# Kernel optimization log

Measured on AMD Instinct MI355X. Metric: run time of the kernel, lower is better.

## Reference

```python
import jax, jax.numpy as jnp
import numpy as np
from jax import lax

T, B, S, D = 16, 8, 256, 1024
M, H = 1024, 8
HD = M // H
TAU_MEM = 0.99
TAU_GATE = 0.9
VTH = 1.0
LN_EPS = 1e-5


def lif(inp, tau, vth):
    """LIF over leading time axis. inp: (T, N, M). Returns (spikes, membrane trace)."""
    def step(v, i):
        v = tau * v + i                      # integrate with leak
        s = (v >= vth).astype(i.dtype)       # hard threshold spike
        return v - s * vth, (s, v)           # subtract reset; trace is pre-reset membrane
    v0 = jnp.zeros(inp.shape[1:], inp.dtype)
    _, (spikes, mv) = lax.scan(step, v0, inp)
    return spikes, mv


def setup_inputs() -> dict:
    key = jax.random.key(0)
    ks = jax.random.split(key, 6)
    inp = {
        "x": jax.random.normal(ks[0], (T, B, S, D), dtype=jnp.float32),
        "W_to_memory": jax.random.normal(ks[1], (M, D), dtype=jnp.float32) / np.sqrt(D),
        "W_gate": jax.random.normal(ks[2], (M, D), dtype=jnp.float32) / np.sqrt(D),
        "W_read_key": jax.random.normal(ks[3], (M, M), dtype=jnp.float32) / np.sqrt(M),
        "W_from_memory": jax.random.normal(ks[4], (D, M), dtype=jnp.float32) / np.sqrt(M),
        "read_query": jax.random.normal(ks[5], (H, HD), dtype=jnp.float32) * 0.02,
        "gate_threshold": jnp.float32(0.5),
        "ln_gamma": jnp.ones((D,), jnp.float32),
        "ln_beta": jnp.zeros((D,), jnp.float32),
        "memory_mix": jnp.float32(0.1),
    }
    return inp


def reference(x, W_to_memory, W_gate, W_read_key, W_from_memory, read_query,
              gate_threshold, ln_gamma, ln_beta, memory_mix):
    N = B * S
    xf = x.reshape(T, N, D)

    # memory write path
    mi = jnp.einsum('tnd,md->tnm', xf, W_to_memory)        # (T,N,M)
    ms, mv = lif(mi, TAU_MEM, VTH)

    # spike-gated write
    gi = jnp.einsum('tnd,md->tnm', xf, W_gate)
    gs, _ = lif(gi, TAU_GATE, VTH)
    gate_sig = gs.mean(axis=0)                              # (N,M)
    gate_mask = jax.nn.sigmoid((gate_sig - gate_threshold) * 10.0)

    # multi-head temporal attention over T
    mvh = mv.reshape(T, N, H, HD)
    mk = jnp.einsum('tnm,km->tnk', mv, W_read_key).reshape(T, N, H, HD)
    scale = 1.0 / np.sqrt(HD)
    attn_s = jnp.einsum('tnhd,hd->tnh', mk, read_query) * scale
    attn_w = jax.nn.softmax(attn_s.astype(jnp.float32), axis=0).astype(mv.dtype)
    mem_read = jnp.einsum('tnhd,tnh->nhd', mvh, attn_w).reshape(N, M)
    mem_read = mem_read * gate_mask

    # project back, layernorm, residual mix
    mem_out = jnp.einsum('nm,dm->nd', mem_read, W_from_memory).astype(jnp.float32)
    mu = mem_out.mean(axis=-1, keepdims=True)
    var = mem_out.var(axis=-1, keepdims=True)
    mem_out = (mem_out - mu) * lax.rsqrt(var + LN_EPS) * ln_gamma + ln_beta
    mem_out = mem_out.astype(x.dtype)

    mix = jax.nn.sigmoid(memory_mix)
    x_enhanced = x + mix * mem_out.reshape(1, B, S, D)
    return x_enhanced
```

## Files before the change

### kernel.cpp

```cpp
#include <hip/hip_runtime.h>
#include <hip/hip_bf16.h>
#include <hip/hip_fp16.h>

#define TT 16
#define NN 2048
#define DD 1024
#define MM 1024
#define HH 8
#define ROWS 32768
#define JJ 2048

typedef _Float16 f16x8 __attribute__((ext_vector_type(8)));
typedef float f32x4 __attribute__((ext_vector_type(4)));

#define SB  __builtin_amdgcn_sched_barrier(0)
#define BAR __builtin_amdgcn_s_barrier()

__device__ __forceinline__ void gload16(const void* g, void* l) {
    __builtin_amdgcn_global_load_lds((const __attribute__((address_space(1))) void*)g,
                                     (__attribute__((address_space(3))) void*)l, 16, 0, 0);
}

__global__ __launch_bounds__(256) void pack_hi(const float* __restrict__ in,
                                               __half* __restrict__ hi, long n4) {
    long i = (long)blockIdx.x * 256 + threadIdx.x;
    if (i >= n4) return;
    float4 v = ((const float4*)in)[i];
    ushort4 H = { __half_as_ushort(__float2half(v.x)), __half_as_ushort(__float2half(v.y)),
                  __half_as_ushort(__float2half(v.z)), __half_as_ushort(__float2half(v.w)) };
    ((ushort4*)hi)[i] = H;
}

__global__ __launch_bounds__(256) void pack_hilo(const float* __restrict__ in,
                                                 __half* __restrict__ hi,
                                                 __half* __restrict__ lo, long n4) {
    long i = (long)blockIdx.x * 256 + threadIdx.x;
    if (i >= n4) return;
    float4 v = ((const float4*)in)[i];
    __half h0 = __float2half(v.x), h1 = __float2half(v.y);
    __half h2 = __float2half(v.z), h3 = __float2half(v.w);
    __half l0 = __float2half(v.x - __half2float(h0));
    __half l1 = __float2half(v.y - __half2float(h1));
    __half l2 = __float2half(v.z - __half2float(h2));
    __half l3 = __float2half(v.w - __half2float(h3));
    ushort4 H = { __half_as_ushort(h0), __half_as_ushort(h1), __half_as_ushort(h2), __half_as_ushort(h3) };
    ushort4 L = { __half_as_ushort(l0), __half_as_ushort(l1), __half_as_ushort(l2), __half_as_ushort(l3) };
    ((ushort4*)hi)[i] = H;
    ((ushort4*)lo)[i] = L;
}

__global__ __launch_bounds__(256) void compute_wq(const float* __restrict__ Wrk,
                                                  const float* __restrict__ q,
                                                  float* __restrict__ wq) {
    int m = blockIdx.x * 256 + threadIdx.x;
    int h = blockIdx.y;
    const float* qh = q + h * 128;
    const float* wr = Wrk + (size_t)h * 128 * MM + m;
    float acc = 0.f;
    for (int hd = 0; hd < 128; hd++) acc = fmaf(qh[hd], wr[(size_t)hd * MM], acc);
    wq[h * MM + m] = acc * 0.08838834764831845f;
}

__global__ __launch_bounds__(512, 2)
void gemm8p(const __half* __restrict__ Ahi, const __half* __restrict__ Alo,
            const __half* __restrict__ Bhi, const __half* __restrict__ Blo,
            float* __restrict__ C)
{
    extern __shared__ __align__(16) char smem[];
    char* AHb = smem;
    char* ALb = smem + 32768;
    char* BHb = smem + 65536;
    char* BLb = smem + 98304;

    const int tid = threadIdx.x, lane = tid & 63, wave = tid >> 6;
    const int l15 = lane & 15, l4 = lane >> 4;
    const int wm = wave >> 2, wn = wave & 3;

    const int orig = blockIdx.x;
    const int wg   = (orig & 7) * 128 + (orig >> 3);
    const int rb   = (wg >> 3) * 256;
    const int cb   = (wg & 7) * 256;

    auto stageU = [&](const __half* src, int row0, char* dstbase, int par, int kt, int s) {
        int t   = s * 512 + tid;
        int row = t >> 2;
        int p   = t & 3;
        int kb  = (p ^ ((row >> 1) & 3)) * 16;
        const char* g = (const char*)(src + (size_t)(row0 + row) * 1024 + kt * 32) + kb;
        gload16(g, dstbase + par * 16384 + (size_t)(s * 512 + wave * 64) * 16);
    };
    auto rdT = [&](const char* base, int par, int row) -> f16x8 {
        int p = l4 ^ ((row >> 1) & 3);
        return *(const f16x8*)(base + par * 16384 + row * 64 + p * 16);
    };

    f32x4 acc[8][4] = {};
    const int NKT = 32;

    stageU(Ahi, rb, AHb, 0, 0, 0); stageU(Ahi, rb, AHb, 0, 0, 1);
    stageU(Alo, rb, ALb, 0, 0, 0); stageU(Alo, rb, ALb, 0, 0, 1);
    stageU(Bhi, cb, BHb, 0, 0, 0); stageU(Bhi, cb, BHb, 0, 0, 1);
    stageU(Blo, cb, BLb, 0, 0, 0); stageU(Blo, cb, BLb, 0, 0, 1);

    for (int kt = 0; kt < NKT; kt++) {
        const int p = kt & 1, pn = p ^ 1;
        const bool pre = (kt + 1 < NKT);
        f16x8 a[8], bh[4], bl[4];

        asm volatile("s_waitcnt vmcnt(0)" ::: "memory");
        SB; BAR;

        #pragma unroll
        for (int i = 0; i < 8; i++) a[i] = rdT(AHb, p, wm * 128 + i * 16 + l15);
        #pragma unroll
        for (int n = 0; n < 4; n++) bh[n] = rdT(BHb, p, wn * 64 + n * 16 + l15);
        if (pre) {
            stageU(Ahi, rb, AHb, pn, kt + 1, 0); stageU(Ahi, rb, AHb, pn, kt + 1, 1);
            stageU(Alo, rb, ALb, pn, kt + 1, 0); stageU(Alo, rb, ALb, pn, kt + 1, 1);
        }
        __builtin_amdgcn_s_setprio(1);
        #pragma unroll
        for (int i = 0; i < 8; i++)
            #pragma unroll
            for (int n = 0; n < 4; n++)
                acc[i][n] = __builtin_amdgcn_mfma_f32_16x16x32_f16(a[i], bh[n], acc[i][n], 0, 0, 0);
        __builtin_amdgcn_s_setprio(0);

        #pragma unroll
        for (int n = 0; n < 4; n++) bl[n] = rdT(BLb, p, wn * 64 + n * 16 + l15);
        if (pre) {
            stageU(Bhi, cb, BHb, pn, kt + 1, 0); stageU(Bhi, cb, BHb, pn, kt + 1, 1);
            stageU(Blo, cb, BLb, pn, kt + 1, 0); stageU(Blo, cb, BLb, pn, kt + 1, 1);
        }
        __builtin_amdgcn_s_setprio(1);
        #pragma unroll
        for (int i = 0; i < 8; i++)
            #pragma unroll
            for (int n = 0; n < 4; n++)
                acc[i][n] = __builtin_amdgcn_mfma_f32_16x16x32_f16(a[i], bl[n], acc[i][n], 0, 0, 0);
        __builtin_amdgcn_s_setprio(0);

        #pragma unroll
        for (int i = 0; i < 8; i++) a[i] = rdT(ALb, p, wm * 128 + i * 16 + l15);
        __builtin_amdgcn_s_setprio(1);
        #pragma unroll
        for (int i = 0; i < 8; i++)
            #pragma unroll
            for (int n = 0; n < 4; n++)
                acc[i][n] = __builtin_amdgcn_mfma_f32_16x16x32_f16(a[i], bh[n], acc[i][n], 0, 0, 0);
        __builtin_amdgcn_s_setprio(0);
    }

    #pragma unroll
    for (int i = 0; i < 8; i++) {
        int r0 = rb + wm * 128 + i * 16 + l4 * 4;
        #pragma unroll
        for (int nf = 0; nf < 4; nf++) {
            int c = cb + wn * 64 + nf * 16 + l15;
            #pragma unroll
            for (int reg = 0; reg < 4; reg++)
                C[(size_t)(r0 + reg) * JJ + c] = acc[i][nf][reg];
        }
    }
}

template<int TERMS>
__global__ __launch_bounds__(256, 2)
void gemm_f16(const __half* __restrict__ Ahi, const __half* __restrict__ Alo,
              const __half* __restrict__ Bhi, const __half* __restrict__ Blo,
              float* __restrict__ C, int K, int ldc, int ncb_log2)
{
    __shared__ __align__(16) __half lds[2][4][8][512];
    const int tid  = threadIdx.x;
    const int lane = tid & 63;
    const int wave = tid >> 6;
    const int l15  = lane & 15, l4 = lane >> 4;

    const int nwg  = gridDim.x;
    const int orig = blockIdx.x;
    const int wg   = (orig & 7) * (nwg >> 3) + (orig >> 3);
    const int rb = (wg >> ncb_log2) * 128;
    const int cb = (wg & ((1 << ncb_log2) - 1)) * 128;

    auto stage = [&](int buf, int ks) {
        const int k0 = ks * 32;
        #pragma unroll
        for (int qq = 0; qq < 2; qq++) {
            int g = wave * 2 + qq;
            size_t aoff = (size_t)(rb + g * 16 + l15) * K + (k0 + 8 * l4);
            gload16(Ahi + aoff, &lds[buf][0][g][0]);
            if constexpr (TERMS == 3) gload16(Alo + aoff, &lds[buf][1][g][0]);
            size_t boff = (size_t)(cb + g * 16 + l15) * K + (k0 + 8 * l4);
            gload16(Bhi + boff, &lds[buf][2][g][0]);
            if constexpr (TERMS == 3) gload16(Blo + boff, &lds[buf][3][g][0]);
        }
    };

    const int wave_r = (wave >> 1) * 64;
    const int wave_c = (wave & 1) * 64;
    const int ag0 = wave_r >> 4;
    const int bg0 = wave_c >> 4;

    f32x4 acc[4][4] = {};
    const int nks = K >> 5;
    stage(0, 0);
    int buf = 0;
    for (int ks = 0; ks < nks; ks++) {
        __syncthreads();
        if (ks + 1 < nks) stage(buf ^ 1, ks + 1);
        f16x8 ah[4], bh[4], al[4], bl[4];
        #pragma unroll
        for (int i = 0; i < 4; i++) {
            ah[i] = *(const f16x8*)&lds[buf][0][ag0 + i][lane * 8];
            bh[i] = *(const f16x8*)&lds[buf][2][bg0 + i][lane * 8];
            if constexpr (TERMS == 3) {
                al[i] = *(const f16x8*)&lds[buf][1][ag0 + i][lane * 8];
                bl[i] = *(const f16x8*)&lds[buf][3][bg0 + i][lane * 8];
            }
        }
        #pragma unroll
        for (int m = 0; m < 4; m++)
            #pragma unroll
            for (int n = 0; n < 4; n++) {
                acc[m][n] = __builtin_amdgcn_mfma_f32_16x16x32_f16(ah[m], bh[n], acc[m][n], 0, 0, 0);
                if constexpr (TERMS == 3) {
                    acc[m][n] = __builtin_amdgcn_mfma_f32_16x16x32_f16(ah[m], bl[n], acc[m][n], 0, 0, 0);
                    acc[m][n] = __builtin_amdgcn_mfma_f32_16x16x32_f16(al[m], bh[n], acc[m][n], 0, 0, 0);
                }
            }
        buf ^= 1;
    }
    #pragma unroll
    for (int m = 0; m < 4; m++)
        #pragma unroll
        for (int n = 0; n < 4; n++) {
            int r0 = rb + wave_r + m * 16 + l4 * 4;
            int c  = cb + wave_c + n * 16 + l15;
            #pragma unroll
            for (int reg = 0; reg < 4; reg++)
                C[(size_t)(r0 + reg) * ldc + c] = acc[m][n][reg];
        }
}

__global__ __launch_bounds__(256)
void lif_kernel(const float* __restrict__ mi_gi, __half* __restrict__ mv,
                float* __restrict__ gmask, const float* __restrict__ gate_thr)
{
    int idx = blockIdx.x * 256 + threadIdx.x;
    int n = idx >> 10, m = idx & 1023;
    const float* pm = mi_gi + (size_t)n * JJ + m;
    const size_t tstride = (size_t)NN * JJ;
    __half* pv = mv + idx;
    float vm = 0.f, vg = 0.f, cnt = 0.f;
    #pragma unroll
    for (int t = 0; t < TT; t++) {
        float im = pm[(size_t)t * tstride];
        vm = 0.99f * vm + im;
        pv[(size_t)t * (NN * MM)] = __float2half(vm);
        if (vm >= 1.0f) vm -= 1.0f;
        float ig = pm[(size_t)t * tstride + MM];
        vg = 0.9f * vg + ig;
        if (vg >= 1.0f) { vg -= 1.0f; cnt += 1.0f; }
    }
    float gs = cnt * 0.0625f;
    gmask[idx] = 1.0f / (1.0f + expf(-10.0f * (gs - gate_thr[0])));
}

__global__ __launch_bounds__(256)
void attn_memread(const __half* __restrict__ mv, const float* __restrict__ wq,
                  const float* __restrict__ gmask, __half* __restrict__ mem_read)
{
    int n = blockIdx.x;
    __shared__ __align__(16) __half smv[TT][1032];
    __shared__ float sw[HH][TT];
    __shared__ float ssm[HH][TT];
    int tid = threadIdx.x;

    for (int t = 0; t < TT; t++) {
        const ushort4* src = (const ushort4*)(mv + ((size_t)t * NN + n) * MM);
        ((ushort4*)&smv[t][0])[tid] = src[tid];
    }
    __syncthreads();

    if (tid < 128) {
        int h = tid >> 4, t = tid & 15;
        const float* w = wq + h * MM;
        float acc = 0.f;
        for (int m = 0; m < MM; m += 2) {
            float2 v = __half22float2(*(const __half2*)&smv[t][m]);
            acc = fmaf(v.x, w[m], acc);
            acc = fmaf(v.y, w[m + 1], acc);
        }
        sw[h][t] = acc;
    }
    __syncthreads();
    if (tid < 8) {
        int h = tid;
        float mx = -1e30f;
        for (int t = 0; t < TT; t++) mx = fmaxf(mx, sw[h][t]);
        float s = 0.f;
        for (int t = 0; t < TT; t++) { float e = __expf(sw[h][t] - mx); ssm[h][t] = e; s += e; }
        float inv = 1.0f / s;
        for (int t = 0; t < TT; t++) ssm[h][t] *= inv;
    }
    __syncthreads();

    const float* gm = gmask + (size_t)n * MM;
    #pragma unroll
    for (int mm = 0; mm < 4; mm++) {
        int m = tid + mm * 256;
        int h = m >> 7;
        float acc = 0.f;
        #pragma unroll
        for (int t = 0; t < TT; t++) acc = fmaf(__half2float(smv[t][m]), ssm[h][t], acc);
        acc *= gm[m];
        mem_read[(size_t)n * MM + m] = __float2half(acc);
    }
}

__global__ __launch_bounds__(256)
void ln_add(const float* __restrict__ mem_out, const float* __restrict__ x,
            const float* __restrict__ gamma, const float* __restrict__ beta,
            const float* __restrict__ mmix, float* __restrict__ out)
{
    int n = blockIdx.x, tid = threadIdx.x;
    int lane = tid & 63, wave = tid >> 6;
    __shared__ float sred[10];
    float4 v = ((const float4*)(mem_out + (size_t)n * DD))[tid];
    float s  = v.x + v.y + v.z + v.w;
    float ss = v.x * v.x + v.y * v.y + v.z * v.z + v.w * v.w;
    #pragma unroll
    for (int o = 32; o > 0; o >>= 1) { s += __shfl_down(s, o, 64); ss += __shfl_down(ss, o, 64); }
    if (lane == 0) { sred[wave * 2] = s; sred[wave * 2 + 1] = ss; }
    __syncthreads();
    if (tid == 0) {
        float S = 0.f, SS = 0.f;
        for (int w = 0; w < 4; w++) { S += sred[w * 2]; SS += sred[w * 2 + 1]; }
        float mu = S * (1.0f / DD);
        float var = SS * (1.0f / DD) - mu * mu;
        sred[8] = mu;
        sred[9] = rsqrtf(var + 1e-5f);
    }
    __syncthreads();
    float mu = sred[8], rs = sred[9];
    float4 g = ((const float4*)gamma)[tid];
    float4 b = ((const float4*)beta)[tid];
    float4 nv;
    nv.x = (v.x - mu) * rs * g.x + b.x;
    nv.y = (v.y - mu) * rs * g.y + b.y;
    nv.z = (v.z - mu) * rs * g.z + b.z;
    nv.w = (v.w - mu) * rs * g.w + b.w;
    float mix = 1.0f / (1.0f + expf(-mmix[0]));
    for (int t = 0; t < TT; t++) {
        size_t off = ((size_t)t * NN + n) * DD;
        float4 xv = ((const float4*)(x + off))[tid];
        float4 o;
        o.x = xv.x + mix * nv.x;
        o.y = xv.y + mix * nv.y;
        o.z = xv.z + mix * nv.z;
        o.w = xv.w + mix * nv.w;
        ((float4*)(out + off))[tid] = o;
    }
}

__global__ void ws_sentinel(float* out) { out[0] = 12345.0f; }

extern "C" void kernel_launch(void* const* d_in, const int* in_sizes, int n_in,
                              void* d_out, int out_size, void* d_ws, size_t ws_size,
                              hipStream_t stream)
{
    const float* x     = (const float*)d_in[0];
    const float* Wto   = (const float*)d_in[1];
    const float* Wg    = (const float*)d_in[2];
    const float* Wrk   = (const float*)d_in[3];
    const float* Wfrom = (const float*)d_in[4];
    const float* q     = (const float*)d_in[5];
    const float* gthr  = (const float*)d_in[6];
    const float* gamma = (const float*)d_in[7];
    const float* beta  = (const float*)d_in[8];
    const float* mmix  = (const float*)d_in[9];
    float* out = (float*)d_out;

    char* w = (char*)d_ws;
    size_t off = 0;
    auto alloc = [&](size_t bytes) -> void* {
        void* p = w + off;
        off += (bytes + 255) & ~(size_t)255;
        return p;
    };
    __half* x_hi   = (__half*)alloc((size_t)ROWS * DD * 2);
    __half* x_lo   = (__half*)alloc((size_t)ROWS * DD * 2);
    __half* wc_hi  = (__half*)alloc((size_t)JJ * DD * 2);
    __half* wc_lo  = (__half*)alloc((size_t)JJ * DD * 2);
    __half* wf_hi  = (__half*)alloc((size_t)DD * MM * 2);
    float*  wq     = (float*) alloc((size_t)HH * MM * 4);
    float*  mi_gi  = (float*) alloc((size_t)ROWS * JJ * 4);
    __half* mv     = (__half*)alloc((size_t)TT * NN * MM * 2);
    float*  gmask  = (float*) alloc((size_t)NN * MM * 4);
    __half* m_read = (__half*)alloc((size_t)NN * MM * 2);
    float*  m_out  = (float*) alloc((size_t)NN * DD * 4);

    if (off > ws_size) {
        ws_sentinel<<<1, 1, 0, stream>>>(out);
        return;
    }

    hipFuncSetAttribute((const void*)gemm8p, hipFuncAttributeMaxDynamicSharedMemorySize, 131072);

    pack_hilo<<<(ROWS * DD / 4 + 255) / 256, 256, 0, stream>>>(x, x_hi, x_lo, ROWS * DD / 4);
    pack_hilo<<<(MM * DD / 4 + 255) / 256, 256, 0, stream>>>(Wto, wc_hi, wc_lo, MM * DD / 4);
    pack_hilo<<<(MM * DD / 4 + 255) / 256, 256, 0, stream>>>(Wg, wc_hi + (size_t)MM * DD, wc_lo + (size_t)MM * DD, MM * DD / 4);
    pack_hi<<<(DD * MM / 4 + 255) / 256, 256, 0, stream>>>(Wfrom, wf_hi, DD * MM / 4);
    compute_wq<<<dim3(4, 8), 256, 0, stream>>>(Wrk, q, wq);

    gemm8p<<<(ROWS / 256) * (JJ / 256), 512, 131072, stream>>>(x_hi, x_lo, wc_hi, wc_lo, mi_gi);

    lif_kernel<<<NN * MM / 256, 256, 0, stream>>>(mi_gi, mv, gmask, gthr);

    attn_memread<<<NN, 256, 0, stream>>>(mv, wq, gmask, m_read);

    gemm_f16<1><<<(NN / 128) * (DD / 128), 256, 0, stream>>>(m_read, m_read, wf_hi, wf_hi, m_out, MM, DD, 3);

    ln_add<<<NN, 256, 0, stream>>>(m_out, x, gamma, beta, mmix, out);
}
```

Measured before the change: 583.8 us.

## Fuse LIF scan into GEMM epilogue via time-permuted row packing

The x packing now permutes rows so that each 256-row GEMM tile holds all 16 timesteps of 16 tokens, laid out to match the MFMA accumulator register pattern. The GEMM epilogue then runs the membrane and gate LIF recurrences in registers. It stages mv through LDS for coalesced fp16 stores and writes the gate mask directly. This removes the 256MB fp32 mi_gi intermediate and the separate LIF kernel's full read pass, in exchange for a heavier epilogue with serial per-thread recurrences and an extra barrier.

Measured after the change: 506.0 us. 1.15x faster.

```diff
diff --git a/kernel.cpp b/kernel.cpp
--- a/kernel.cpp
+++ b/kernel.cpp
@@ -49,6 +49,30 @@
     ((ushort4*)lo)[i] = L;
 }
 
+__global__ __launch_bounds__(256) void pack_hilo_perm(const float* __restrict__ in,
+                                                      __half* __restrict__ hi,
+                                                      __half* __restrict__ lo) {
+    long i = (long)blockIdx.x * 256 + threadIdx.x;
+    int R   = (int)(i >> 8);
+    int d4  = (int)(i & 255);
+    int r   = R & 255, blk = R >> 8;
+    int n_l = ((r >> 7) & 1) * 8 + ((r >> 6) & 1) * 4 + ((r >> 2) & 3);
+    int t   = ((r >> 4) & 3) * 4 + (r & 3);
+    int n_g = blk * 16 + n_l;
+    long src = ((long)t * NN + n_g) * 256 + d4;
+    float4 v = ((const float4*)in)[src];
+    __half h0 = __float2half(v.x), h1 = __float2half(v.y);
+    __half h2 = __float2half(v.z), h3 = __float2half(v.w);
+    __half l0 = __float2half(v.x - __half2float(h0));
+    __half l1 = __float2half(v.y - __half2float(h1));
+    __half l2 = __float2half(v.z - __half2float(h2));
+    __half l3 = __float2half(v.w - __half2float(h3));
+    ushort4 H = { __half_as_ushort(h0), __half_as_ushort(h1), __half_as_ushort(h2), __half_as_ushort(h3) };
+    ushort4 L = { __half_as_ushort(l0), __half_as_ushort(l1), __half_as_ushort(l2), __half_as_ushort(l3) };
+    ((ushort4*)hi)[i] = H;
+    ((ushort4*)lo)[i] = L;
+}
+
 __global__ __launch_bounds__(256) void compute_wq(const float* __restrict__ Wrk,
                                                   const float* __restrict__ q,
                                                   float* __restrict__ wq) {
@@ -64,7 +88,8 @@
 __global__ __launch_bounds__(512, 2)
 void gemm8p(const __half* __restrict__ Ahi, const __half* __restrict__ Alo,
             const __half* __restrict__ Bhi, const __half* __restrict__ Blo,
-            float* __restrict__ C)
+            __half* __restrict__ mv, float* __restrict__ gmask,
+            const float* __restrict__ gate_thr)
 {
     extern __shared__ __align__(16) char smem[];
     char* AHb = smem;
@@ -151,15 +176,61 @@
         __builtin_amdgcn_s_setprio(0);
     }
 
-    #pragma unroll
-    for (int i = 0; i < 8; i++) {
-        int r0 = rb + wm * 128 + i * 16 + l4 * 4;
-        #pragma unroll
-        for (int nf = 0; nf < 4; nf++) {
-            int c = cb + wn * 64 + nf * 16 + l15;
-            #pragma unroll
-            for (int reg = 0; reg < 4; reg++)
-                C[(size_t)(r0 + reg) * JJ + c] = acc[i][nf][reg];
+    asm volatile("s_waitcnt lgkmcnt(0) vmcnt(0)" ::: "memory");
+    SB; BAR;
+
+    const int n_g_base = rb >> 4;
+    if (cb < 1024) {
+        __half* mvs = (__half*)smem;
+        #pragma unroll
+        for (int i2 = 0; i2 < 2; i2++) {
+            int n_l = wm * 8 + i2 * 4 + l4;
+            #pragma unroll
+            for (int nf = 0; nf < 4; nf++) {
+                int col = wn * 64 + nf * 16 + l15;
+                float v = 0.f;
+                #pragma unroll
+                for (int tt = 0; tt < 4; tt++)
+                    #pragma unroll
+                    for (int reg = 0; reg < 4; reg++) {
+                        int t = tt * 4 + reg;
+                        v = 0.99f * v + acc[i2 * 4 + tt][nf][reg];
+                        mvs[(t * 16 + n_l) * 256 + col] = __float2half(v);
+                        if (v >= 1.0f) v -= 1.0f;
+                    }
+            }
+        }
+        SB; BAR;
+        #pragma unroll
+        for (int j = 0; j < 16; j++) {
+            int k = j * 512 + tid;
+            int e = k * 8;
+            int t   = e >> 12;
+            int n_l = (e >> 8) & 15;
+            int m   = e & 255;
+            float4 val = *(const float4*)((const char*)smem + (size_t)k * 16);
+            *(float4*)(mv + ((size_t)(t * NN + n_g_base + n_l) * MM + cb + m)) = val;
+        }
+    } else {
+        float thr = gate_thr[0];
+        #pragma unroll
+        for (int i2 = 0; i2 < 2; i2++) {
+            int n_l = wm * 8 + i2 * 4 + l4;
+            #pragma unroll
+            for (int nf = 0; nf < 4; nf++) {
+                int col = wn * 64 + nf * 16 + l15;
+                float v = 0.f, cnt = 0.f;
+                #pragma unroll
+                for (int tt = 0; tt < 4; tt++)
+                    #pragma unroll
+                    for (int reg = 0; reg < 4; reg++) {
+                        v = 0.9f * v + acc[i2 * 4 + tt][nf][reg];
+                        if (v >= 1.0f) { v -= 1.0f; cnt += 1.0f; }
+                    }
+                float gs = cnt * 0.0625f;
+                gmask[(size_t)(n_g_base + n_l) * MM + (cb - 1024) + col] =
+                    1.0f / (1.0f + expf(-10.0f * (gs - thr)));
+            }
         }
     }
 }
@@ -240,30 +311,6 @@
             for (int reg = 0; reg < 4; reg++)
                 C[(size_t)(r0 + reg) * ldc + c] = acc[m][n][reg];
         }
-}
-
-__global__ __launch_bounds__(256)
-void lif_kernel(const float* __restrict__ mi_gi, __half* __restrict__ mv,
-                float* __restrict__ gmask, const float* __restrict__ gate_thr)
-{
-    int idx = blockIdx.x * 256 + threadIdx.x;
-    int n = idx >> 10, m = idx & 1023;
-    const float* pm = mi_gi + (size_t)n * JJ + m;
-    const size_t tstride = (size_t)NN * JJ;
-    __half* pv = mv + idx;
-    float vm = 0.f, vg = 0.f, cnt = 0.f;
-    #pragma unroll
-    for (int t = 0; t < TT; t++) {
-        float im = pm[(size_t)t * tstride];
-        vm = 0.99f * vm + im;
-        pv[(size_t)t * (NN * MM)] = __float2half(vm);
-        if (vm >= 1.0f) vm -= 1.0f;
-        float ig = pm[(size_t)t * tstride + MM];
-        vg = 0.9f * vg + ig;
-        if (vg >= 1.0f) { vg -= 1.0f; cnt += 1.0f; }
-    }
-    float gs = cnt * 0.0625f;
-    gmask[idx] = 1.0f / (1.0f + expf(-10.0f * (gs - gate_thr[0])));
 }
 
 __global__ __launch_bounds__(256)
@@ -394,7 +441,6 @@
     __half* wc_lo  = (__half*)alloc((size_t)JJ * DD * 2);
     __half* wf_hi  = (__half*)alloc((size_t)DD * MM * 2);
     float*  wq     = (float*) alloc((size_t)HH * MM * 4);
-    float*  mi_gi  = (float*) alloc((size_t)ROWS * JJ * 4);
     __half* mv     = (__half*)alloc((size_t)TT * NN * MM * 2);
     float*  gmask  = (float*) alloc((size_t)NN * MM * 4);
     __half* m_read = (__half*)alloc((size_t)NN * MM * 2);
@@ -407,15 +453,13 @@
 
     hipFuncSetAttribute((const void*)gemm8p, hipFuncAttributeMaxDynamicSharedMemorySize, 131072);
 
-    pack_hilo<<<(ROWS * DD / 4 + 255) / 256, 256, 0, stream>>>(x, x_hi, x_lo, ROWS * DD / 4);
+    pack_hilo_perm<<<ROWS * DD / 4 / 256, 256, 0, stream>>>(x, x_hi, x_lo);
     pack_hilo<<<(MM * DD / 4 + 255) / 256, 256, 0, stream>>>(Wto, wc_hi, wc_lo, MM * DD / 4);
     pack_hilo<<<(MM * DD / 4 + 255) / 256, 256, 0, stream>>>(Wg, wc_hi + (size_t)MM * DD, wc_lo + (size_t)MM * DD, MM * DD / 4);
     pack_hi<<<(DD * MM / 4 + 255) / 256, 256, 0, stream>>>(Wfrom, wf_hi, DD * MM / 4);
     compute_wq<<<dim3(4, 8), 256, 0, stream>>>(Wrk, q, wq);
 
-    gemm8p<<<(ROWS / 256) * (JJ / 256), 512, 131072, stream>>>(x_hi, x_lo, wc_hi, wc_lo, mi_gi);
-
-    lif_kernel<<<NN * MM / 256, 256, 0, stream>>>(mi_gi, mv, gmask, gthr);
+    gemm8p<<<(ROWS / 256) * (JJ / 256), 512, 131072, stream>>>(x_hi, x_lo, wc_hi, wc_lo, mv, gmask, gthr);
 
     attn_memread<<<NN, 256, 0, stream>>>(mv, wq, gmask, m_read);
 
```
